# Optimization experiments

Hardware: AMD Instinct MI355X
Metric: run time of the kernel (lower is better)

## Reference

```python
import jax, jax.numpy as jnp
import numpy as np

B, S, D, H, KD = 4, 2048, 640, 10, 64


def setup_inputs() -> dict:
    key = jax.random.key(0)
    k0, k1, k2, k3, k4 = jax.random.split(key, 5)
    x = jax.random.normal(k0, (B, S, D), dtype=jnp.float32)
    # per-head projection weights, stacked over heads: [H, D, KD]
    Wq = jax.random.normal(k1, (H, D, KD), dtype=jnp.float32) * 0.05
    Wk = jax.random.normal(k2, (H, D, KD), dtype=jnp.float32) * 0.05
    Wv = jax.random.normal(k3, (H, D, KD), dtype=jnp.float32) * 0.05
    # output projection: [H*KD, D]
    Wo = jax.random.normal(k4, (H * KD, D), dtype=jnp.float32) * 0.05
    return {"x": x, "Wq": Wq, "Wk": Wk, "Wv": Wv, "Wo": Wo}


def reference(x, Wq, Wk, Wv, Wo):
    # Batched equivalent of the per-head Python loop:
    # each head computes q=x@Wq_h, k=x@Wk_h, v=x@Wv_h, softmax(q k^T / sqrt(KD)) @ v
    q = jnp.einsum("bsd,hdk->bhsk", x, Wq)
    k = jnp.einsum("bsd,hdk->bhsk", x, Wk)
    v = jnp.einsum("bsd,hdk->bhsk", x, Wv)
    scale = 1.0 / jnp.sqrt(jnp.asarray(KD, x.dtype))
    scores = jnp.einsum("bhsk,bhtk->bhst", q, k) * scale  # [B,H,S,S]
    attn = jax.nn.softmax(scores, axis=-1)
    z = jnp.einsum("bhst,bhtk->bhsk", attn, v)  # [B,H,S,KD]
    # concat heads along last axis (head 0 first, matching the loop order)
    z = z.transpose(0, 2, 1, 3).reshape(x.shape[0], x.shape[1], H * KD)
    return jnp.einsum("bsf,fd->bsd", z, Wo)
```

## Files before the change

kernel.cpp:

```cpp
#include <hip/hip_runtime.h>
#include <hip/hip_bf16.h>

#define B_  4
#define S_  2048
#define D_  640
#define H_  10
#define KD_ 64

typedef __attribute__((ext_vector_type(8))) short  short8;
typedef __attribute__((ext_vector_type(4))) short  short4v;
typedef __attribute__((ext_vector_type(4))) float  floatx4;
typedef __attribute__((ext_vector_type(2))) unsigned int uint2v;

static __device__ __forceinline__ short f2bf_fast(float f) {
    unsigned int u = __float_as_uint(f);
    u += 0x7fffu + ((u >> 16) & 1u);
    return (short)(u >> 16);
}
static __device__ __forceinline__ unsigned int pack2bf(float a, float b) {
    union { __hip_bfloat162 h; unsigned int u; } c;
    c.h = __float22bfloat162_rn(float2{a, b});
    return c.u;
}

static __device__ __forceinline__ void gload_lds16(const void* gp, void* lp) {
    __builtin_amdgcn_global_load_lds(
        (const __attribute__((address_space(1))) unsigned int*)gp,
        (__attribute__((address_space(3))) unsigned int*)lp, 16, 0, 0);
}

__global__ __launch_bounds__(256) void prep(
        const float* __restrict__ x,
        const float* __restrict__ Wq, const float* __restrict__ Wk,
        const float* __restrict__ Wv, const float* __restrict__ Wo,
        short* __restrict__ xb, short* __restrict__ BigT,
        short* __restrict__ WoT) {
    __shared__ float tile[32][33];
    int bid = blockIdx.x;
    if (bid < 5120) {
        int idx = (bid * 256 + threadIdx.x) * 4;
        float4 v = *(const float4*)(x + idx);
        uint2v o;
        o[0] = pack2bf(v.x, v.y);
        o[1] = pack2bf(v.z, v.w);
        *(uint2v*)(xb + idx) = o;
    } else if (bid < 6320) {
        int flat = bid - 5120;
        int bz = flat / 40, rem = flat % 40;
        int by = rem >> 1, bxx = rem & 1;
        int w = bz / 10, h = bz % 10;
        const float* W = ((w == 0) ? Wq : (w == 1) ? Wk : Wv) + h * 640 * 64;
        short* out = BigT + (w * 640 + h * 64) * 640;
        int c0 = bxx * 32;
        int r0 = by * 32;
        int tx = threadIdx.x & 31, ty = threadIdx.x >> 5;
        #pragma unroll
        for (int k = 0; k < 4; ++k)
            tile[ty + 8 * k][tx] = W[(r0 + ty + 8 * k) * 64 + c0 + tx];
        __syncthreads();
        #pragma unroll
        for (int k = 0; k < 4; ++k)
            out[(c0 + ty + 8 * k) * 640 + r0 + tx] = f2bf_fast(tile[tx][ty + 8 * k]);
    } else {
        int flat = bid - 6320;
        int c0 = (flat % 20) * 32;
        int r0 = (flat / 20) * 32;
        int tx = threadIdx.x & 31, ty = threadIdx.x >> 5;
        #pragma unroll
        for (int k = 0; k < 4; ++k)
            tile[ty + 8 * k][tx] = Wo[(r0 + ty + 8 * k) * 640 + c0 + tx];
        __syncthreads();
        #pragma unroll
        for (int k = 0; k < 4; ++k)
            WoT[(c0 + ty + 8 * k) * 640 + r0 + tx] = f2bf_fast(tile[tx][ty + 8 * k]);
    }
}


__global__ __launch_bounds__(256) void qkv_gemm(
        const short* __restrict__ X, const short* __restrict__ BigT,
        short* __restrict__ qb, short* __restrict__ kb, short* __restrict__ vtb) {
    __shared__ __align__(16) short Ab[2][128][32];
    __shared__ __align__(16) short Bb[2][128][32];

    int wave = threadIdx.x >> 6;
    int lane = threadIdx.x & 63;
    int lq = lane & 15, quad = lane >> 4;
    int wm = (wave & 1) * 64, wn = (wave >> 1) * 64;

    int lin = blockIdx.y * 64 + blockIdx.x;
    int tm = ((lin & 7) * 8 + ((lin >> 3) & 7)) * 128;
    int tn = (lin >> 6) * 128;

    int srow = lane >> 2;
    int schunk = (lane & 3) ^ ((lane >> 3) & 3);
    const short* Asrc0 = X    + (tm + wave * 32 + srow) * 640 + schunk * 8;
    const short* Bsrc0 = BigT + (tn + wave * 32 + srow) * 640 + schunk * 8;
    const short* Asrc1 = Asrc0 + 16 * 640;
    const short* Bsrc1 = Bsrc0 + 16 * 640;

    floatx4 acc[4][4];
    for (int a = 0; a < 4; ++a)
        for (int n = 0; n < 4; ++n)
            acc[a][n] = (floatx4){0.f, 0.f, 0.f, 0.f};

    int rsw = (lq >> 1) & 3;

    gload_lds16(Asrc0, &Ab[0][wave * 32][0]);
    gload_lds16(Asrc1, &Ab[0][wave * 32 + 16][0]);
    gload_lds16(Bsrc0, &Bb[0][wave * 32][0]);
    gload_lds16(Bsrc1, &Bb[0][wave * 32 + 16][0]);

    int p = 0;
    bool isV = (tn >= 1280);

    for (int k0 = 0; k0 < 640; k0 += 32) {
        __syncthreads();
        if (k0 + 32 < 640) {
            int pn = p ^ 1;
            gload_lds16(Asrc0 + k0 + 32, &Ab[pn][wave * 32][0]);
            gload_lds16(Asrc1 + k0 + 32, &Ab[pn][wave * 32 + 16][0]);
            gload_lds16(Bsrc0 + k0 + 32, &Bb[pn][wave * 32][0]);
            gload_lds16(Bsrc1 + k0 + 32, &Bb[pn][wave * 32 + 16][0]);
        }

        short8 af[4], bf[4];
        #pragma unroll
        for (int t = 0; t < 4; ++t) {
            af[t] = *(const short8*)(&Ab[p][wm + t * 16 + lq][(quad ^ rsw) * 8]);
            bf[t] = *(const short8*)(&Bb[p][wn + t * 16 + lq][(quad ^ rsw) * 8]);
        }
        if (!isV) {
            #pragma unroll
            for (int mt = 0; mt < 4; ++mt)
                #pragma unroll
                for (int nt = 0; nt < 4; ++nt)
                    acc[mt][nt] = __builtin_amdgcn_mfma_f32_16x16x32_bf16(
                        af[mt], bf[nt], acc[mt][nt], 0, 0, 0);
        } else {
            #pragma unroll
            for (int nt = 0; nt < 4; ++nt)
                #pragma unroll
                for (int mt = 0; mt < 4; ++mt)
                    acc[nt][mt] = __builtin_amdgcn_mfma_f32_16x16x32_bf16(
                        bf[nt], af[mt], acc[nt][mt], 0, 0, 0);
        }
        p ^= 1;
    }

    if (!isV) {
        const float qscale = 0.18033688011112042f;
        short* dst = (tn < 640) ? qb : kb;
        float scale = (tn < 640) ? qscale : 1.0f;
        #pragma unroll
        for (int nt = 0; nt < 4; ++nt) {
            int rem = (tn + wn + nt * 16) % 640;
            int hh = rem / 64, kd = (rem % 64) + lq;
            #pragma unroll
            for (int mt = 0; mt < 4; ++mt) {
                #pragma unroll
                for (int r = 0; r < 4; ++r) {
                    int m = tm + wm + mt * 16 + quad * 4 + r;
                    int b = m >> 11, s = m & 2047;
                    dst[((b * H_ + hh) * S_ + s) * KD_ + kd] =
                        f2bf_fast(acc[mt][nt][r] * scale);
                }
            }
        }
    } else {
        #pragma unroll
        for (int nt = 0; nt < 4; ++nt) {
            int rem = (tn + wn + nt * 16) - 1280;
            int hh = rem / 64;
            int kd0 = (rem % 64) + quad * 4;
            #pragma unroll
            for (int mt = 0; mt < 4; ++mt) {
                int m = tm + wm + mt * 16 + lq;
                int b = m >> 11, s = m & 2047;
                #pragma unroll
                for (int r = 0; r < 4; ++r) {
                    vtb[((b * H_ + hh) * KD_ + kd0 + r) * S_ + s] =
                        f2bf_fast(acc[nt][mt][r]);
                }
            }
        }
    }
}

__global__ __launch_bounds__(256, 3) void attn(
        const short* __restrict__ qb, const short* __restrict__ kbuf,
        const short* __restrict__ vtb, short* __restrict__ zb) {
    __shared__ __align__(16) short Kbuf[3][64][64];
    __shared__ __align__(16) short Vbuf[3][64][64];

    int wave = threadIdx.x >> 6;
    int lane = threadIdx.x & 63;
    int lq = lane & 15, quad = lane >> 4;

    int bx = blockIdx.x;
    int xcd = bx & 7, slot = bx >> 3;
    int bh = xcd * 5 + (slot >> 4);
    int qt = slot & 15;
    int b = bh / 10, h = bh % 10;
    int q0 = qt * 128;

    const short* qp = qb + (b * H_ + h) * S_ * KD_;
    const short* kp = kbuf + (b * H_ + h) * S_ * KD_;
    const short* vp = vtb + (b * H_ + h) * KD_ * S_;

    int r8 = lane >> 3;
    int g  = (lane & 7) ^ r8;
    const short* kg0 = kp + (wave * 16 + r8) * 64 + g * 8;
    const short* kg1 = kp + (wave * 16 + 8 + r8) * 64 + g * 8;
    const short* vg0 = vp + (wave * 16 + r8) * (long)S_ + g * 8;
    const short* vg1 = vp + (wave * 16 + 8 + r8) * (long)S_ + g * 8;

    short8 qA0, qA1, qB0, qB1;
    {
        int rowA = q0 + wave * 32 + lq;
        qA0 = *(const short8*)(qp + rowA * 64 + quad * 8);
        qA1 = *(const short8*)(qp + rowA * 64 + 32 + quad * 8);
        qB0 = *(const short8*)(qp + (rowA + 16) * 64 + quad * 8);
        qB1 = *(const short8*)(qp + (rowA + 16) * 64 + 32 + quad * 8);
    }

    short8 ones;
    #pragma unroll
    for (int i = 0; i < 8; ++i) ones[i] = (short)0x3F80;

    floatx4 OA[4], OB[4];
    for (int n = 0; n < 4; ++n) {
        OA[n] = (floatx4){0.f, 0.f, 0.f, 0.f};
        OB[n] = (floatx4){0.f, 0.f, 0.f, 0.f};
    }
    floatx4 lsvA = (floatx4){0.f, 0.f, 0.f, 0.f};
    floatx4 lsvB = (floatx4){0.f, 0.f, 0.f, 0.f};

    int sw = lq & 7;

    #define STAGE_KV(tt, bi) do { \
        gload_lds16(kg0 + (tt) * 4096, &Kbuf[bi][wave * 16][0]); \
        gload_lds16(kg1 + (tt) * 4096, &Kbuf[bi][wave * 16 + 8][0]); \
        gload_lds16(vg0 + (tt) * 64,   &Vbuf[bi][wave * 16][0]); \
        gload_lds16(vg1 + (tt) * 64,   &Vbuf[bi][wave * 16 + 8][0]); \
    } while (0)

    auto compute_tile = [&](int bi) {
        const short* Kb = &Kbuf[bi][0][0];
        const short* Vb = &Vbuf[bi][0][0];

        floatx4 sTA[4], sTB[4];
        __builtin_amdgcn_s_setprio(1);
        #pragma unroll
        for (int kblk = 0; kblk < 4; ++kblk) {
            const short* krow = Kb + (kblk * 16 + lq) * 64;
            short8 bk0 = *(const short8*)(krow + (quad ^ sw) * 8);
            short8 bk1 = *(const short8*)(krow + ((quad + 4) ^ sw) * 8);
            floatx4 zA = (floatx4){0.f, 0.f, 0.f, 0.f};
            zA = __builtin_amdgcn_mfma_f32_16x16x32_bf16(bk0, qA0, zA, 0, 0, 0);
            sTA[kblk] = __builtin_amdgcn_mfma_f32_16x16x32_bf16(bk1, qA1, zA, 0, 0, 0);
            floatx4 zB = (floatx4){0.f, 0.f, 0.f, 0.f};
            zB = __builtin_amdgcn_mfma_f32_16x16x32_bf16(bk0, qB0, zB, 0, 0, 0);
            sTB[kblk] = __builtin_amdgcn_mfma_f32_16x16x32_bf16(bk1, qB1, zB, 0, 0, 0);
        }
        __builtin_amdgcn_s_setprio(0);

        #pragma unroll
        for (int ts = 0; ts < 2; ++ts) {
            int ka = ts * 2, kc = ts * 2 + 1;
            unsigned int a00 = pack2bf(__builtin_amdgcn_exp2f(sTA[ka][0]),
                                       __builtin_amdgcn_exp2f(sTA[ka][1]));
            unsigned int a01 = pack2bf(__builtin_amdgcn_exp2f(sTA[ka][2]),
                                       __builtin_amdgcn_exp2f(sTA[ka][3]));
            unsigned int a10 = pack2bf(__builtin_amdgcn_exp2f(sTA[kc][0]),
                                       __builtin_amdgcn_exp2f(sTA[kc][1]));
            unsigned int a11 = pack2bf(__builtin_amdgcn_exp2f(sTA[kc][2]),
                                       __builtin_amdgcn_exp2f(sTA[kc][3]));
            uint2v sa0 = __builtin_amdgcn_permlane32_swap(a00, a10, false, false);
            uint2v sa1 = __builtin_amdgcn_permlane32_swap(a01, a11, false, false);
            uint2v wa02 = __builtin_amdgcn_permlane16_swap(sa0[0], sa0[1], false, false);
            uint2v wa13 = __builtin_amdgcn_permlane16_swap(sa1[0], sa1[1], false, false);
            union { unsigned int u[4]; short8 s8; } pfa;
            pfa.u[0] = wa02[0];
            pfa.u[1] = wa13[0];
            pfa.u[2] = wa02[1];
            pfa.u[3] = wa13[1];
            short8 pfA = pfa.s8;
            unsigned int b00 = pack2bf(__builtin_amdgcn_exp2f(sTB[ka][0]),
                                       __builtin_amdgcn_exp2f(sTB[ka][1]));
            unsigned int b01 = pack2bf(__builtin_amdgcn_exp2f(sTB[ka][2]),
                                       __builtin_amdgcn_exp2f(sTB[ka][3]));
            unsigned int b10 = pack2bf(__builtin_amdgcn_exp2f(sTB[kc][0]),
                                       __builtin_amdgcn_exp2f(sTB[kc][1]));
            unsigned int b11 = pack2bf(__builtin_amdgcn_exp2f(sTB[kc][2]),
                                       __builtin_amdgcn_exp2f(sTB[kc][3]));
            uint2v sb0 = __builtin_amdgcn_permlane32_swap(b00, b10, false, false);
            uint2v sb1 = __builtin_amdgcn_permlane32_swap(b01, b11, false, false);
            uint2v wb02 = __builtin_amdgcn_permlane16_swap(sb0[0], sb0[1], false, false);
            uint2v wb13 = __builtin_amdgcn_permlane16_swap(sb1[0], sb1[1], false, false);
            union { unsigned int u[4]; short8 s8; } pfb;
            pfb.u[0] = wb02[0];
            pfb.u[1] = wb13[0];
            pfb.u[2] = wb02[1];
            pfb.u[3] = wb13[1];
            short8 pfB = pfb.s8;

            __builtin_amdgcn_s_setprio(1);
            lsvA = __builtin_amdgcn_mfma_f32_16x16x32_bf16(ones, pfA, lsvA, 0, 0, 0);
            lsvB = __builtin_amdgcn_mfma_f32_16x16x32_bf16(ones, pfB, lsvB, 0, 0, 0);
            #pragma unroll
            for (int db = 0; db < 4; ++db) {
                const short* vrow = Vb + (db * 16 + lq) * 64;
                short8 bv = *(const short8*)(vrow + ((ts * 4 + quad) ^ sw) * 8);
                OA[db] = __builtin_amdgcn_mfma_f32_16x16x32_bf16(bv, pfA, OA[db], 0, 0, 0);
                OB[db] = __builtin_amdgcn_mfma_f32_16x16x32_bf16(bv, pfB, OB[db], 0, 0, 0);
            }
            __builtin_amdgcn_s_setprio(0);
        }
    };

    STAGE_KV(0, 0);
    STAGE_KV(1, 1);

    int bi = 0;
    for (int t = 0; t < 30; ++t) {
        asm volatile("s_waitcnt vmcnt(4)\n\ts_barrier" ::: "memory");
        int bn = bi + 2;
        if (bn >= 3) bn -= 3;
        STAGE_KV(t + 2, bn);
        compute_tile(bi);
        ++bi;
        if (bi == 3) bi = 0;
    }
    asm volatile("s_waitcnt vmcnt(4)\n\ts_barrier" ::: "memory");
    compute_tile(bi);
    ++bi;
    if (bi == 3) bi = 0;
    asm volatile("s_waitcnt vmcnt(0)\n\ts_barrier" ::: "memory");
    compute_tile(bi);

    #undef STAGE_KV

    float invA = 1.0f / lsvA[0];
    float invB = 1.0f / lsvB[0];

    int sA = q0 + wave * 32 + lq;
    int sB = sA + 16;
    short* zrA = zb + (b * S_ + sA) * 640 + h * 64;
    short* zrB = zb + (b * S_ + sB) * 640 + h * 64;
    #pragma unroll
    for (int db = 0; db < 4; ++db) {
        uint2v za, zv;
        za[0] = pack2bf(OA[db][0] * invA, OA[db][1] * invA);
        za[1] = pack2bf(OA[db][2] * invA, OA[db][3] * invA);
        *(uint2v*)(zrA + db * 16 + quad * 4) = za;
        zv[0] = pack2bf(OB[db][0] * invB, OB[db][1] * invB);
        zv[1] = pack2bf(OB[db][2] * invB, OB[db][3] * invB);
        *(uint2v*)(zrB + db * 16 + quad * 4) = zv;
    }
}

__global__ __launch_bounds__(256) void out_gemm(
        const short* __restrict__ Z, const short* __restrict__ WoT,
        float* __restrict__ out) {
    __shared__ __align__(16) short Ab[2][128][32];
    __shared__ __align__(16) short Bb[2][64][32];

    int wave = threadIdx.x >> 6;
    int lane = threadIdx.x & 63;
    int lq = lane & 15, quad = lane >> 4;
    int wm = (wave & 1) * 64;
    int wn = (wave >> 1) * 32;

    int lin = blockIdx.y * 64 + blockIdx.x;
    int tm = ((lin & 7) * 8 + ((lin >> 3) & 7)) * 128;
    int tn = (lin >> 6) * 64;

    int srow = lane >> 2;
    int schunk = (lane & 3) ^ ((lane >> 3) & 3);
    const short* Asrc0 = Z   + (tm + wave * 32 + srow) * 640 + schunk * 8;
    const short* Asrc1 = Asrc0 + 16 * 640;
    const short* Bsrc0 = WoT + (tn + wave * 16 + srow) * 640 + schunk * 8;

    floatx4 acc[4][2];
    for (int a = 0; a < 4; ++a)
        for (int n = 0; n < 2; ++n)
            acc[a][n] = (floatx4){0.f, 0.f, 0.f, 0.f};

    int rsw = (lq >> 1) & 3;

    gload_lds16(Asrc0, &Ab[0][wave * 32][0]);
    gload_lds16(Asrc1, &Ab[0][wave * 32 + 16][0]);
    gload_lds16(Bsrc0, &Bb[0][wave * 16][0]);

    int p = 0;
    for (int k0 = 0; k0 < 640; k0 += 32) {
        __syncthreads();
        if (k0 + 32 < 640) {
            int pn = p ^ 1;
            gload_lds16(Asrc0 + k0 + 32, &Ab[pn][wave * 32][0]);
            gload_lds16(Asrc1 + k0 + 32, &Ab[pn][wave * 32 + 16][0]);
            gload_lds16(Bsrc0 + k0 + 32, &Bb[pn][wave * 16][0]);
        }

        short8 af[4], bf[2];
        #pragma unroll
        for (int t = 0; t < 4; ++t)
            af[t] = *(const short8*)(&Ab[p][wm + t * 16 + lq][(quad ^ rsw) * 8]);
        #pragma unroll
        for (int u = 0; u < 2; ++u)
            bf[u] = *(const short8*)(&Bb[p][wn + u * 16 + lq][(quad ^ rsw) * 8]);
        #pragma unroll
        for (int mt = 0; mt < 4; ++mt)
            #pragma unroll
            for (int nt = 0; nt < 2; ++nt)
                acc[mt][nt] = __builtin_amdgcn_mfma_f32_16x16x32_bf16(
                    af[mt], bf[nt], acc[mt][nt], 0, 0, 0);
        p ^= 1;
    }

    #pragma unroll
    for (int mt = 0; mt < 4; ++mt) {
        #pragma unroll
        for (int nt = 0; nt < 2; ++nt) {
            #pragma unroll
            for (int r = 0; r < 4; ++r) {
                int m = tm + wm + mt * 16 + quad * 4 + r;
                out[m * 640 + tn + wn + nt * 16 + lq] = acc[mt][nt][r];
            }
        }
    }
}

extern "C" void kernel_launch(void* const* d_in, const int* in_sizes, int n_in,
                              void* d_out, int out_size, void* d_ws, size_t ws_size,
                              hipStream_t stream) {
    const float* x  = (const float*)d_in[0];
    const float* Wq = (const float*)d_in[1];
    const float* Wk = (const float*)d_in[2];
    const float* Wv = (const float*)d_in[3];
    const float* Wo = (const float*)d_in[4];
    float* out = (float*)d_out;

    char* ws = (char*)d_ws;
    short* BigT = (short*)(ws);
    short* WoT  = (short*)(ws + 2457600);
    short* xb   = (short*)(ws + 3276800);
    short* qb   = (short*)(ws + 13762560);
    short* kb   = (short*)(ws + 24248320);
    short* vtb  = (short*)(ws + 34734080);
    short* zb   = (short*)(ws + 45219840);

    prep<<<dim3(6720), dim3(256), 0, stream>>>(x, Wq, Wk, Wv, Wo, xb, BigT, WoT);
    qkv_gemm<<<dim3(64, 15), dim3(256), 0, stream>>>(xb, BigT, qb, kb, vtb);
    attn<<<dim3(640), dim3(256), 0, stream>>>(qb, kb, vtb, zb);
    out_gemm<<<dim3(64, 10), dim3(256), 0, stream>>>(zb, WoT, out);
}
```

Measured before the change: 190.4 us.

## Switch attention kernel to 32x32x16 MFMA tiles

Rewrites the attention inner loop to use 32x32x16 bf16 MFMA instructions in place of 16x16x32 ones, covering each wave's 32 query rows in one tile instead of two. This changes the register layout of the Q fragments, score tiles and output accumulators, and simplifies the P relayout to only permlane32 swaps. The aim is fewer MFMA issues, fewer LDS reads of K and V fragments and less permute work per tile, at the cost of larger accumulator vectors and longer per-instruction latency.

```diff
diff --git a/kernel.cpp b/kernel.cpp
--- a/kernel.cpp
+++ b/kernel.cpp
@@ -10,6 +10,7 @@
 typedef __attribute__((ext_vector_type(8))) short  short8;
 typedef __attribute__((ext_vector_type(4))) short  short4v;
 typedef __attribute__((ext_vector_type(4))) float  floatx4;
+typedef __attribute__((ext_vector_type(16))) float floatx16;
 typedef __attribute__((ext_vector_type(2))) unsigned int uint2v;
 
 static __device__ __forceinline__ short f2bf_fast(float f) {
@@ -195,7 +196,8 @@
 
     int wave = threadIdx.x >> 6;
     int lane = threadIdx.x & 63;
-    int lq = lane & 15, quad = lane >> 4;
+    int q = lane & 31;
+    int hi = lane >> 5;
 
     int bx = blockIdx.x;
     int xcd = bx & 7, slot = bx >> 3;
@@ -209,34 +211,29 @@
     const short* vp = vtb + (b * H_ + h) * KD_ * S_;
 
     int r8 = lane >> 3;
-    int g  = (lane & 7) ^ r8;
-    const short* kg0 = kp + (wave * 16 + r8) * 64 + g * 8;
-    const short* kg1 = kp + (wave * 16 + 8 + r8) * 64 + g * 8;
-    const short* vg0 = vp + (wave * 16 + r8) * (long)S_ + g * 8;
-    const short* vg1 = vp + (wave * 16 + 8 + r8) * (long)S_ + g * 8;
-
-    short8 qA0, qA1, qB0, qB1;
+    int g  = (lane & 7) ^ (r8 & 7);
+    const short* kg0 = kp + (wave * 16 + (lane >> 3)) * 64 + g * 8;
+    const short* kg1 = kp + (wave * 16 + 8 + (lane >> 3)) * 64 + g * 8;
+    const short* vg0 = vp + (wave * 16 + (lane >> 3)) * (long)S_ + g * 8;
+    const short* vg1 = vp + (wave * 16 + 8 + (lane >> 3)) * (long)S_ + g * 8;
+
+    short8 qf[4];
     {
-        int rowA = q0 + wave * 32 + lq;
-        qA0 = *(const short8*)(qp + rowA * 64 + quad * 8);
-        qA1 = *(const short8*)(qp + rowA * 64 + 32 + quad * 8);
-        qB0 = *(const short8*)(qp + (rowA + 16) * 64 + quad * 8);
-        qB1 = *(const short8*)(qp + (rowA + 16) * 64 + 32 + quad * 8);
+        int qrow = q0 + wave * 32 + q;
+        #pragma unroll
+        for (int c = 0; c < 4; ++c)
+            qf[c] = *(const short8*)(qp + qrow * 64 + c * 16 + hi * 8);
     }
 
     short8 ones;
     #pragma unroll
     for (int i = 0; i < 8; ++i) ones[i] = (short)0x3F80;
 
-    floatx4 OA[4], OB[4];
-    for (int n = 0; n < 4; ++n) {
-        OA[n] = (floatx4){0.f, 0.f, 0.f, 0.f};
-        OB[n] = (floatx4){0.f, 0.f, 0.f, 0.f};
-    }
-    floatx4 lsvA = (floatx4){0.f, 0.f, 0.f, 0.f};
-    floatx4 lsvB = (floatx4){0.f, 0.f, 0.f, 0.f};
-
-    int sw = lq & 7;
+    floatx16 O0, O1, lsv;
+    #pragma unroll
+    for (int i = 0; i < 16; ++i) { O0[i] = 0.f; O1[i] = 0.f; lsv[i] = 0.f; }
+
+    int sw7 = q & 7;
 
     #define STAGE_KV(tt, bi) do { \
         gload_lds16(kg0 + (tt) * 4096, &Kbuf[bi][wave * 16][0]); \
@@ -245,78 +242,53 @@
         gload_lds16(vg1 + (tt) * 64,   &Vbuf[bi][wave * 16 + 8][0]); \
     } while (0)
 
+    #define CHUNK(SRC, CC, C) do { \
+        unsigned int w0_ = pack2bf(__builtin_amdgcn_exp2f(SRC[8 * (CC) + 0]), \
+                                   __builtin_amdgcn_exp2f(SRC[8 * (CC) + 1])); \
+        unsigned int w1_ = pack2bf(__builtin_amdgcn_exp2f(SRC[8 * (CC) + 2]), \
+                                   __builtin_amdgcn_exp2f(SRC[8 * (CC) + 3])); \
+        unsigned int w2_ = pack2bf(__builtin_amdgcn_exp2f(SRC[8 * (CC) + 4]), \
+                                   __builtin_amdgcn_exp2f(SRC[8 * (CC) + 5])); \
+        unsigned int w3_ = pack2bf(__builtin_amdgcn_exp2f(SRC[8 * (CC) + 6]), \
+                                   __builtin_amdgcn_exp2f(SRC[8 * (CC) + 7])); \
+        uint2v t_ = __builtin_amdgcn_permlane32_swap(w0_, w2_, false, false); \
+        uint2v u_ = __builtin_amdgcn_permlane32_swap(w1_, w3_, false, false); \
+        union { unsigned int u[4]; short8 s8; } pf_; \
+        pf_.u[0] = t_[0]; pf_.u[1] = u_[0]; \
+        pf_.u[2] = t_[1]; pf_.u[3] = u_[1]; \
+        short8 pf = pf_.s8; \
+        int jl_ = ((2 * (C) + hi) ^ sw7) * 8; \
+        short8 va_ = *(const short8*)(Vb + q * 64 + jl_); \
+        short8 vb_ = *(const short8*)(Vb + (32 + q) * 64 + jl_); \
+        __builtin_amdgcn_s_setprio(1); \
+        lsv = __builtin_amdgcn_mfma_f32_32x32x16_bf16(ones, pf, lsv, 0, 0, 0); \
+        O0 = __builtin_amdgcn_mfma_f32_32x32x16_bf16(va_, pf, O0, 0, 0, 0); \
+        O1 = __builtin_amdgcn_mfma_f32_32x32x16_bf16(vb_, pf, O1, 0, 0, 0); \
+        __builtin_amdgcn_s_setprio(0); \
+    } while (0)
+
     auto compute_tile = [&](int bi) {
         const short* Kb = &Kbuf[bi][0][0];
         const short* Vb = &Vbuf[bi][0][0];
 
-        floatx4 sTA[4], sTB[4];
+        floatx16 sT0, sT1;
+        #pragma unroll
+        for (int i = 0; i < 16; ++i) { sT0[i] = 0.f; sT1[i] = 0.f; }
         __builtin_amdgcn_s_setprio(1);
         #pragma unroll
-        for (int kblk = 0; kblk < 4; ++kblk) {
-            const short* krow = Kb + (kblk * 16 + lq) * 64;
-            short8 bk0 = *(const short8*)(krow + (quad ^ sw) * 8);
-            short8 bk1 = *(const short8*)(krow + ((quad + 4) ^ sw) * 8);
-            floatx4 zA = (floatx4){0.f, 0.f, 0.f, 0.f};
-            zA = __builtin_amdgcn_mfma_f32_16x16x32_bf16(bk0, qA0, zA, 0, 0, 0);
-            sTA[kblk] = __builtin_amdgcn_mfma_f32_16x16x32_bf16(bk1, qA1, zA, 0, 0, 0);
-            floatx4 zB = (floatx4){0.f, 0.f, 0.f, 0.f};
-            zB = __builtin_amdgcn_mfma_f32_16x16x32_bf16(bk0, qB0, zB, 0, 0, 0);
-            sTB[kblk] = __builtin_amdgcn_mfma_f32_16x16x32_bf16(bk1, qB1, zB, 0, 0, 0);
+        for (int c = 0; c < 4; ++c) {
+            int jl = ((2 * c + hi) ^ sw7) * 8;
+            short8 ka = *(const short8*)(Kb + q * 64 + jl);
+            short8 kb2 = *(const short8*)(Kb + (32 + q) * 64 + jl);
+            sT0 = __builtin_amdgcn_mfma_f32_32x32x16_bf16(ka, qf[c], sT0, 0, 0, 0);
+            sT1 = __builtin_amdgcn_mfma_f32_32x32x16_bf16(kb2, qf[c], sT1, 0, 0, 0);
         }
         __builtin_amdgcn_s_setprio(0);
 
-        #pragma unroll
-        for (int ts = 0; ts < 2; ++ts) {
-            int ka = ts * 2, kc = ts * 2 + 1;
-            unsigned int a00 = pack2bf(__builtin_amdgcn_exp2f(sTA[ka][0]),
-                                       __builtin_amdgcn_exp2f(sTA[ka][1]));
-            unsigned int a01 = pack2bf(__builtin_amdgcn_exp2f(sTA[ka][2]),
-                                       __builtin_amdgcn_exp2f(sTA[ka][3]));
-            unsigned int a10 = pack2bf(__builtin_amdgcn_exp2f(sTA[kc][0]),
-                                       __builtin_amdgcn_exp2f(sTA[kc][1]));
-            unsigned int a11 = pack2bf(__builtin_amdgcn_exp2f(sTA[kc][2]),
-                                       __builtin_amdgcn_exp2f(sTA[kc][3]));
-            uint2v sa0 = __builtin_amdgcn_permlane32_swap(a00, a10, false, false);
-            uint2v sa1 = __builtin_amdgcn_permlane32_swap(a01, a11, false, false);
-            uint2v wa02 = __builtin_amdgcn_permlane16_swap(sa0[0], sa0[1], false, false);
-            uint2v wa13 = __builtin_amdgcn_permlane16_swap(sa1[0], sa1[1], false, false);
-            union { unsigned int u[4]; short8 s8; } pfa;
-            pfa.u[0] = wa02[0];
-            pfa.u[1] = wa13[0];
-            pfa.u[2] = wa02[1];
-            pfa.u[3] = wa13[1];
-            short8 pfA = pfa.s8;
-            unsigned int b00 = pack2bf(__builtin_amdgcn_exp2f(sTB[ka][0]),
-                                       __builtin_amdgcn_exp2f(sTB[ka][1]));
-            unsigned int b01 = pack2bf(__builtin_amdgcn_exp2f(sTB[ka][2]),
-                                       __builtin_amdgcn_exp2f(sTB[ka][3]));
-            unsigned int b10 = pack2bf(__builtin_amdgcn_exp2f(sTB[kc][0]),
-                                       __builtin_amdgcn_exp2f(sTB[kc][1]));
-            unsigned int b11 = pack2bf(__builtin_amdgcn_exp2f(sTB[kc][2]),
-                                       __builtin_amdgcn_exp2f(sTB[kc][3]));
-            uint2v sb0 = __builtin_amdgcn_permlane32_swap(b00, b10, false, false);
-            uint2v sb1 = __builtin_amdgcn_permlane32_swap(b01, b11, false, false);
-            uint2v wb02 = __builtin_amdgcn_permlane16_swap(sb0[0], sb0[1], false, false);
-            uint2v wb13 = __builtin_amdgcn_permlane16_swap(sb1[0], sb1[1], false, false);
-            union { unsigned int u[4]; short8 s8; } pfb;
-            pfb.u[0] = wb02[0];
-            pfb.u[1] = wb13[0];
-            pfb.u[2] = wb02[1];
-            pfb.u[3] = wb13[1];
-            short8 pfB = pfb.s8;
-
-            __builtin_amdgcn_s_setprio(1);
-            lsvA = __builtin_amdgcn_mfma_f32_16x16x32_bf16(ones, pfA, lsvA, 0, 0, 0);
-            lsvB = __builtin_amdgcn_mfma_f32_16x16x32_bf16(ones, pfB, lsvB, 0, 0, 0);
-            #pragma unroll
-            for (int db = 0; db < 4; ++db) {
-                const short* vrow = Vb + (db * 16 + lq) * 64;
-                short8 bv = *(const short8*)(vrow + ((ts * 4 + quad) ^ sw) * 8);
-                OA[db] = __builtin_amdgcn_mfma_f32_16x16x32_bf16(bv, pfA, OA[db], 0, 0, 0);
-                OB[db] = __builtin_amdgcn_mfma_f32_16x16x32_bf16(bv, pfB, OB[db], 0, 0, 0);
-            }
-            __builtin_amdgcn_s_setprio(0);
-        }
+        CHUNK(sT0, 0, 0);
+        CHUNK(sT0, 1, 1);
+        CHUNK(sT1, 0, 2);
+        CHUNK(sT1, 1, 3);
     };
 
     STAGE_KV(0, 0);
@@ -340,23 +312,22 @@
     compute_tile(bi);
 
     #undef STAGE_KV
-
-    float invA = 1.0f / lsvA[0];
-    float invB = 1.0f / lsvB[0];
-
-    int sA = q0 + wave * 32 + lq;
-    int sB = sA + 16;
-    short* zrA = zb + (b * S_ + sA) * 640 + h * 64;
-    short* zrB = zb + (b * S_ + sB) * 640 + h * 64;
+    #undef CHUNK
+
+    float inv = 1.0f / lsv[0];
+
+    int s = q0 + wave * 32 + q;
+    short* zr = zb + (b * S_ + s) * 640 + h * 64;
     #pragma unroll
-    for (int db = 0; db < 4; ++db) {
-        uint2v za, zv;
-        za[0] = pack2bf(OA[db][0] * invA, OA[db][1] * invA);
-        za[1] = pack2bf(OA[db][2] * invA, OA[db][3] * invA);
-        *(uint2v*)(zrA + db * 16 + quad * 4) = za;
-        zv[0] = pack2bf(OB[db][0] * invB, OB[db][1] * invB);
-        zv[1] = pack2bf(OB[db][2] * invB, OB[db][3] * invB);
-        *(uint2v*)(zrB + db * 16 + quad * 4) = zv;
+    for (int rq = 0; rq < 4; ++rq) {
+        int kd0 = 8 * rq + 4 * hi;
+        uint2v w0, w1;
+        w0[0] = pack2bf(O0[4 * rq + 0] * inv, O0[4 * rq + 1] * inv);
+        w0[1] = pack2bf(O0[4 * rq + 2] * inv, O0[4 * rq + 3] * inv);
+        *(uint2v*)(zr + kd0) = w0;
+        w1[0] = pack2bf(O1[4 * rq + 0] * inv, O1[4 * rq + 1] * inv);
+        w1[1] = pack2bf(O1[4 * rq + 2] * inv, O1[4 * rq + 3] * inv);
+        *(uint2v*)(zr + 32 + kd0) = w1;
     }
 }
 
```

Result: no change. 190.7 us (+0.2%).
